# Kernel tuning notes

Hardware: AMD Instinct MI355X
Metric: run time of the kernel (lower is better)

Reference implementation:

```python
import jax, jax.numpy as jnp
import numpy as np


def l2norm(t, eps=1e-12):
    return t / jnp.clip(jnp.linalg.norm(t, axis=-1, keepdims=True), eps, None)


def setup_inputs() -> dict:
    key = jax.random.key(0)
    k1, k2 = jax.random.split(key)
    x = jax.random.normal(k1, (16, 2048, 512), dtype=jnp.float32)
    # codebook: module inits with l2norm(uniform_init(...)); random normals then l2norm is equivalent in spirit
    embed = l2norm(jax.random.normal(k2, (1, 8192, 512), dtype=jnp.float32))
    return {"x": x, "embed": embed}


def reference(x, embed):
    # x: [b, n, d] (ndim < 4 -> add codebook dim h=1), embed: [h, c, d]
    xh = x[None]                                  # [1, b, n, d]
    h, b, n, d = xh.shape
    flatten = l2norm(xh.reshape(h, b * n, d))     # [h, bn, d]
    embed_n = l2norm(embed)                       # [h, c, d]
    # cosine-similarity distances
    dist = jnp.einsum('hnd,hcd->hnc', flatten, embed_n)   # [h, bn, c]
    # sample_codebook_temp = 0 -> gumbel_sample degenerates to argmax
    embed_ind = jnp.argmax(dist, axis=-1).reshape(h, b, n)  # [h, b, n]
    # batched_embedding: gather from the UN-normalized codebook
    quantize = jnp.take_along_axis(embed[:, None], embed_ind[..., None, None].repeat(1, 0), axis=2) if False else embed[jnp.arange(h)[:, None, None], embed_ind]  # [h, b, n, d]
    return quantize[0], embed_ind[0]
```

## Files before the change

### kernel.cpp

```cpp
#include <hip/hip_runtime.h>
#include <math.h>

#define D 512
#define MROWS 32768
#define CCOLS 8192
#define K2 1536
#define NT 24
#define NSPLIT 2
#define CT_PER_SPLIT 16
#define SUBT_PER_CTI (NT * 2)
#define SUBT_TOTAL (CT_PER_SPLIT * SUBT_PER_CTI)
#define TAU 2.0e-4f

typedef __attribute__((ext_vector_type(8))) short short8v;
typedef __attribute__((ext_vector_type(4))) float f32x4;

__device__ __forceinline__ unsigned short f2bf_rne(float f) {
    unsigned u = __float_as_uint(f);
    unsigned r = ((u >> 16) & 1u) + 0x7FFFu;
    return (unsigned short)((u + r) >> 16);
}
__device__ __forceinline__ float bf2f(unsigned short h) {
    return __uint_as_float(((unsigned)h) << 16);
}

__device__ __forceinline__ void gload_lds16(const void* gsrc, void* ldst) {
    __builtin_amdgcn_global_load_lds(
        (const __attribute__((address_space(1))) unsigned int*)gsrc,
        (__attribute__((address_space(3))) unsigned int*)ldst, 16, 0, 0);
}

__global__ __launch_bounds__(64) void prep_embed_kernel(
    const float* __restrict__ embed, unsigned short* __restrict__ E2,
    float* __restrict__ inv_norm) {
    int cb = blockIdx.x, lane = threadIdx.x;
    const float4* r4 = reinterpret_cast<const float4*>(embed + (size_t)cb * D);
    float4 a = r4[lane], b = r4[lane + 64];
    float ss = a.x*a.x + a.y*a.y + a.z*a.z + a.w*a.w
             + b.x*b.x + b.y*b.y + b.z*b.z + b.w*b.w;
#pragma unroll
    for (int off = 32; off > 0; off >>= 1) ss += __shfl_xor(ss, off);
    float inv = 1.0f / fmaxf(sqrtf(ss), 1e-12f);
    if (lane == 0) inv_norm[cb] = inv;
    float ea[4] = {a.x*inv, a.y*inv, a.z*inv, a.w*inv};
    float eb[4] = {b.x*inv, b.y*inv, b.z*inv, b.w*inv};
    ushort4 ha, la, hb, lb;
    { for (int j=0;j<4;++j) (&ha.x)[j] = f2bf_rne(ea[j]); }
    { for (int j=0;j<4;++j) (&la.x)[j] = f2bf_rne(ea[j] - bf2f((&ha.x)[j])); }
    { for (int j=0;j<4;++j) (&hb.x)[j] = f2bf_rne(eb[j]); }
    { for (int j=0;j<4;++j) (&lb.x)[j] = f2bf_rne(eb[j] - bf2f((&hb.x)[j])); }
    unsigned short* row = E2 + (size_t)cb * K2;
    int k = lane * 4;
    *(ushort4*)&row[k]          = ha;
    *(ushort4*)&row[256 + k]    = hb;
    *(ushort4*)&row[512 + k]    = la;
    *(ushort4*)&row[768 + k]    = lb;
    *(ushort4*)&row[1024 + k]   = ha;
    *(ushort4*)&row[1280 + k]   = hb;
}

__global__ __launch_bounds__(64) void prep_x_kernel(
    const float* __restrict__ x, unsigned short* __restrict__ X2) {
    int rb = blockIdx.x, lane = threadIdx.x;
    const float4* r4 = reinterpret_cast<const float4*>(x + (size_t)rb * D);
    float4 a = r4[lane], b = r4[lane + 64];
    float ea[4] = {a.x, a.y, a.z, a.w};
    float eb[4] = {b.x, b.y, b.z, b.w};
    ushort4 ha, la, hb, lb;
    { for (int j=0;j<4;++j) (&ha.x)[j] = f2bf_rne(ea[j]); }
    { for (int j=0;j<4;++j) (&la.x)[j] = f2bf_rne(ea[j] - bf2f((&ha.x)[j])); }
    { for (int j=0;j<4;++j) (&hb.x)[j] = f2bf_rne(eb[j]); }
    { for (int j=0;j<4;++j) (&lb.x)[j] = f2bf_rne(eb[j] - bf2f((&hb.x)[j])); }
    unsigned short* row = X2 + (size_t)rb * K2;
    int k = lane * 4;
    *(ushort4*)&row[k]        = ha;
    *(ushort4*)&row[256 + k]  = hb;
    *(ushort4*)&row[512 + k]  = ha;
    *(ushort4*)&row[768 + k]  = hb;
    *(ushort4*)&row[1024 + k] = la;
    *(ushort4*)&row[1280 + k] = lb;
}

__global__ __launch_bounds__(512, 2) void gemm_topk5_kernel(
    const unsigned short* __restrict__ X2, const unsigned short* __restrict__ E2,
    float4* __restrict__ partials) {
    __shared__ __align__(16) unsigned short AsR[4][256 * 32];
    __shared__ __align__(16) unsigned short BsR[4][256 * 32];
    __shared__ float smv1[256], smv2[256];
    __shared__ int   smi[256];

    const int tid  = threadIdx.x;
    const int lane = tid & 63;
    const int w    = tid >> 6;
    const int wm   = w >> 1;
    const int wn   = w & 1;
    const int c    = lane & 15;
    const int qh   = lane >> 4;

    const int bid     = blockIdx.x;
    const int logical = (bid & 7) * 32 + (bid >> 3);
    const int split   = logical >> 7;
    const int rowtile = logical & 127;
    const size_t grow0 = (size_t)rowtile * 256;
    const int col0     = split * (CT_PER_SPLIT * 256);

    float v1[16], v2[16]; int i1[16];
#pragma unroll
    for (int s = 0; s < 16; ++s) { v1[s] = -3.0e38f; v2[s] = -3.0e38f; i1[s] = 0; }

#define STAGE_SUBT(S)                                                         \
    { int cti_ = (S) / SUBT_PER_CTI;                                          \
      int rem_ = (S) - cti_ * SUBT_PER_CTI;                                   \
      int kb_  = (rem_ >> 1) * 64 + (rem_ & 1) * 32;                          \
      int ct_  = col0 + cti_ * 256;                                           \
      int sl_  = (S) & 3;                                                     \
      _Pragma("unroll")                                                       \
      for (int i_ = 0; i_ < 2; ++i_) {                                        \
          int G_ = tid + i_ * 512; int row_ = G_ >> 2;                        \
          int gs_ = (G_ & 3) ^ ((row_ >> 1) & 3);                             \
          gload_lds16(X2 + (grow0 + row_) * (size_t)K2 + kb_ + gs_ * 8,       \
                      &AsR[sl_][G_ * 8]);                                     \
      }                                                                       \
      _Pragma("unroll")                                                       \
      for (int i_ = 0; i_ < 2; ++i_) {                                        \
          int G_ = tid + i_ * 512; int row_ = G_ >> 2;                        \
          int gs_ = (G_ & 3) ^ ((row_ >> 1) & 3);                             \
          gload_lds16(E2 + (size_t)(ct_ + row_) * K2 + kb_ + gs_ * 8,         \
                      &BsR[sl_][G_ * 8]);                                     \
      } }

    STAGE_SUBT(0);
    STAGE_SUBT(1);
    STAGE_SUBT(2);
    asm volatile("s_waitcnt vmcnt(8)" ::: "memory");

    int sgi = 0;
    for (int cti = 0; cti < CT_PER_SPLIT; ++cti) {
        const int ct0 = col0 + cti * 256;
        f32x4 acc[4][8];
#pragma unroll
        for (int m = 0; m < 4; ++m)
#pragma unroll
            for (int n = 0; n < 8; ++n) acc[m][n] = (f32x4){0.f, 0.f, 0.f, 0.f};

#pragma unroll 4
        for (int s = 0; s < SUBT_PER_CTI; ++s, ++sgi) {
            const int slot = sgi & 3;
            __builtin_amdgcn_s_barrier();
            __builtin_amdgcn_sched_barrier(0);

            short8v af[4], bf[4];
#pragma unroll
            for (int m = 0; m < 4; ++m) {
                int row = wm * 64 + m * 16 + c;
                int g   = qh ^ ((row >> 1) & 3);
                af[m] = *(const short8v*)&AsR[slot][row * 32 + g * 8];
            }
#pragma unroll
            for (int n = 0; n < 4; ++n) {
                int rb = wn * 128 + n * 16 + c;
                int g  = qh ^ ((rb >> 1) & 3);
                bf[n] = *(const short8v*)&BsR[slot][rb * 32 + g * 8];
            }
            __builtin_amdgcn_s_setprio(1);
#pragma unroll
            for (int m = 0; m < 4; ++m)
#pragma unroll
                for (int n = 0; n < 4; ++n)
                    acc[m][n] = __builtin_amdgcn_mfma_f32_16x16x32_bf16(
                        af[m], bf[n], acc[m][n], 0, 0, 0);
            __builtin_amdgcn_s_setprio(0);
#pragma unroll
            for (int n = 0; n < 4; ++n) {
                int rb = wn * 128 + (n + 4) * 16 + c;
                int g  = qh ^ ((rb >> 1) & 3);
                bf[n] = *(const short8v*)&BsR[slot][rb * 32 + g * 8];
            }
            __builtin_amdgcn_s_setprio(1);
#pragma unroll
            for (int m = 0; m < 4; ++m)
#pragma unroll
                for (int n = 0; n < 4; ++n)
                    acc[m][n + 4] = __builtin_amdgcn_mfma_f32_16x16x32_bf16(
                        af[m], bf[n], acc[m][n + 4], 0, 0, 0);
            __builtin_amdgcn_s_setprio(0);

            if (sgi + 3 < SUBT_TOTAL) {
                STAGE_SUBT(sgi + 3);
                asm volatile("s_waitcnt vmcnt(8)" ::: "memory");
            } else if (sgi == SUBT_TOTAL - 3) {
                asm volatile("s_waitcnt vmcnt(4)" ::: "memory");
            } else if (sgi == SUBT_TOTAL - 2) {
                asm volatile("s_waitcnt vmcnt(0)" ::: "memory");
            }
        }

#pragma unroll
        for (int m = 0; m < 4; ++m)
#pragma unroll
            for (int n = 0; n < 8; ++n) {
                int col = ct0 + wn * 128 + n * 16 + c;
#pragma unroll
                for (int r = 0; r < 4; ++r) {
                    float sv = acc[m][n][r];
                    int slot2 = m * 4 + r;
                    if (sv > v1[slot2]) { v2[slot2] = v1[slot2]; v1[slot2] = sv; i1[slot2] = col; }
                    else if (sv > v2[slot2]) v2[slot2] = sv;
                }
            }
    }
#undef STAGE_SUBT

#pragma unroll
    for (int s = 0; s < 16; ++s) {
        float a1 = v1[s], a2 = v2[s]; int ai = i1[s];
#pragma unroll
        for (int off = 1; off < 16; off <<= 1) {
            float o1 = __shfl_xor(a1, off);
            float o2 = __shfl_xor(a2, off);
            int   oi = __shfl_xor(ai, off);
            if (o1 > a1 || (o1 == a1 && oi < ai)) {
                a2 = fmaxf(a1, o2); a1 = o1; ai = oi;
            } else {
                a2 = fmaxf(a2, o1);
            }
        }
        v1[s] = a1; v2[s] = a2; i1[s] = ai;
    }
    if (c == 0 && wn == 1) {
#pragma unroll
        for (int s = 0; s < 16; ++s) {
            int li = wm * 64 + qh * 16 + s;
            smv1[li] = v1[s]; smv2[li] = v2[s]; smi[li] = i1[s];
        }
    }
    __syncthreads();
    if (c == 0 && wn == 0) {
#pragma unroll
        for (int s = 0; s < 16; ++s) {
            int li = wm * 64 + qh * 16 + s;
            float o1 = smv1[li], o2 = smv2[li]; int oi = smi[li];
            if (o1 > v1[s] || (o1 == v1[s] && oi < i1[s])) {
                v2[s] = fmaxf(v1[s], o2); v1[s] = o1; i1[s] = oi;
            } else {
                v2[s] = fmaxf(v2[s], o1);
            }
            int row = (int)grow0 + wm * 64 + (s >> 2) * 16 + qh * 4 + (s & 3);
            partials[(size_t)row * 4 + split] =
                make_float4(v1[s], v2[s], __int_as_float(i1[s]), 0.f);
        }
    }
}

__global__ __launch_bounds__(256) void combine_kernel(
    const float4* __restrict__ partials, int* __restrict__ ind,
    int* __restrict__ fb_count, int* __restrict__ fb_rows,
    unsigned long long* __restrict__ best) {
    int row = blockIdx.x * 256 + threadIdx.x;
    if (row >= MROWS) return;
    float g1 = -3.0e38f, g2 = -3.0e38f; int gi = 0;
#pragma unroll
    for (int s = 0; s < NSPLIT; ++s) {
        float4 p = partials[(size_t)row * 4 + s];
        if (p.x > g1 || (p.x == g1 && __float_as_int(p.z) < gi)) {
            g2 = fmaxf(g1, p.y); g1 = p.x; gi = __float_as_int(p.z);
        } else {
            g2 = fmaxf(g2, p.x);
        }
    }
    ind[row] = gi;
    if (g1 - g2 <= TAU) {
        int k = atomicAdd(fb_count, 1);
        fb_rows[k] = row;
        best[row] = 0ull;
    }
}

__global__ __launch_bounds__(256) void fallback_kernel(
    const float* __restrict__ x, const float* __restrict__ embed,
    const float* __restrict__ inv_norm, const int* __restrict__ fb_count,
    const int* __restrict__ fb_rows, unsigned long long* __restrict__ best) {
    __shared__ float es[16][D];
    __shared__ float xs[D];
    const int t = threadIdx.x;
    const int c0 = blockIdx.x * 16;
    for (int i = t; i < 16 * 128; i += 256) {
        int col = i >> 7, f4 = i & 127;
        *(float4*)&es[col][f4 * 4] =
            *(const float4*)&embed[(size_t)(c0 + col) * D + f4 * 4];
    }
    const int nfb = *fb_count;
    const int col = t >> 4, s = t & 15;
    for (int ri = 0; ri < nfb; ++ri) {
        int row = fb_rows[ri];
        __syncthreads();
        if (t < 128)
            *(float4*)&xs[t * 4] = *(const float4*)&x[(size_t)row * D + t * 4];
        __syncthreads();
        float dot = 0.f;
        const float* ep = &es[col][s * 32];
        const float* xp = &xs[s * 32];
#pragma unroll
        for (int k = 0; k < 8; ++k) {
            float4 a = *(const float4*)&xp[k * 4];
            float4 b = *(const float4*)&ep[k * 4];
            dot = fmaf(a.x, b.x, fmaf(a.y, b.y, fmaf(a.z, b.z, fmaf(a.w, b.w, dot))));
        }
        dot += __shfl_xor(dot, 1); dot += __shfl_xor(dot, 2);
        dot += __shfl_xor(dot, 4); dot += __shfl_xor(dot, 8);
        if (s == 0) {
            float score = dot * inv_norm[c0 + col];
            unsigned fb = __float_as_uint(score);
            fb = (fb & 0x80000000u) ? ~fb : (fb | 0x80000000u);
            unsigned long long key = ((unsigned long long)fb << 32) |
                (unsigned long long)(0xFFFFFFFFu - (unsigned)(c0 + col));
            atomicMax(best + row, key);
        }
    }
}

__global__ void fbwrite_kernel(const int* __restrict__ fb_count,
                               const int* __restrict__ fb_rows,
                               const unsigned long long* __restrict__ best,
                               int* __restrict__ ind) {
    int n = *fb_count;
    for (int i = threadIdx.x; i < n; i += 256) {
        int row = fb_rows[i];
        unsigned long long k = best[row];
        ind[row] = (int)(0xFFFFFFFFu - (unsigned)(k & 0xFFFFFFFFull));
    }
}

__global__ __launch_bounds__(128) void gather_kernel(
    const float* __restrict__ embed, const int* __restrict__ ind,
    float* __restrict__ out_q, float* __restrict__ out_i) {
    int row = blockIdx.x;
    int t = threadIdx.x;
    int idx = ind[row];
    const float4* src = reinterpret_cast<const float4*>(embed + (size_t)idx * D);
    float4* dst = reinterpret_cast<float4*>(out_q + (size_t)row * D);
    dst[t] = src[t];
    if (t == 0) out_i[row] = (float)idx;
}

#define BM 64
#define BN 128
#define BK 32
#define LDX (BM + 4)
#define LDE (BN + 4)

__global__ __launch_bounds__(64) void norm_kernel(const float* __restrict__ embed,
                                                  float* __restrict__ inv_norm) {
    int cb = blockIdx.x, lane = threadIdx.x;
    const float4* r4 = reinterpret_cast<const float4*>(embed + (size_t)cb * D);
    float4 a = r4[lane], b = r4[lane + 64];
    float s = a.x*a.x + a.y*a.y + a.z*a.z + a.w*a.w
            + b.x*b.x + b.y*b.y + b.z*b.z + b.w*b.w;
#pragma unroll
    for (int off = 32; off > 0; off >>= 1) s += __shfl_xor(s, off);
    if (lane == 0) inv_norm[cb] = 1.0f / fmaxf(sqrtf(s), 1e-12f);
}

__global__ __launch_bounds__(256) void gemm_argmax_kernel(
    const float* __restrict__ x, const float* __restrict__ embed,
    const float* __restrict__ inv_norm, int* __restrict__ ind, int C) {
    __shared__ float xs[BK][LDX];
    __shared__ float es[BK][LDE];
    const int tid = threadIdx.x;
    const int tx = tid & 15;
    const int ty = tid >> 4;
    const int row0 = blockIdx.x * BM;
    float bestv[4]; int besti[4];
#pragma unroll
    for (int i = 0; i < 4; ++i) { bestv[i] = -3.0e38f; besti[i] = 0; }
    for (int ct = 0; ct < C; ct += BN) {
        float acc[4][8];
#pragma unroll
        for (int i = 0; i < 4; ++i)
#pragma unroll
            for (int j = 0; j < 8; ++j) acc[i][j] = 0.0f;
        for (int kt = 0; kt < D; kt += BK) {
#pragma unroll
            for (int i = 0; i < 2; ++i) {
                int f = tid + i * 256;
                int r = f >> 3, kq = (f & 7) << 2;
                float4 v = *reinterpret_cast<const float4*>(
                    x + (size_t)(row0 + r) * D + kt + kq);
                xs[kq+0][r]=v.x; xs[kq+1][r]=v.y; xs[kq+2][r]=v.z; xs[kq+3][r]=v.w;
            }
#pragma unroll
            for (int i = 0; i < 4; ++i) {
                int f = tid + i * 256;
                int r = f >> 3, kq = (f & 7) << 2;
                float4 v = *reinterpret_cast<const float4*>(
                    embed + (size_t)(ct + r) * D + kt + kq);
                es[kq+0][r]=v.x; es[kq+1][r]=v.y; es[kq+2][r]=v.z; es[kq+3][r]=v.w;
            }
            __syncthreads();
#pragma unroll
            for (int k = 0; k < BK; ++k) {
                float4 a4 = *reinterpret_cast<const float4*>(&xs[k][ty * 4]);
                float4 b0 = *reinterpret_cast<const float4*>(&es[k][tx * 8]);
                float4 b1 = *reinterpret_cast<const float4*>(&es[k][tx * 8 + 4]);
                float a[4] = {a4.x, a4.y, a4.z, a4.w};
                float b[8] = {b0.x, b0.y, b0.z, b0.w, b1.x, b1.y, b1.z, b1.w};
#pragma unroll
                for (int i = 0; i < 4; ++i)
#pragma unroll
                    for (int j = 0; j < 8; ++j)
                        acc[i][j] = fmaf(a[i], b[j], acc[i][j]);
            }
            __syncthreads();
        }
#pragma unroll
        for (int i = 0; i < 4; ++i) {
            float v = -3.0e38f; int vi = 0;
#pragma unroll
            for (int j = 0; j < 8; ++j) {
                int col = ct + tx * 8 + j;
                float s = acc[i][j] * inv_norm[col];
                if (s > v) { v = s; vi = col; }
            }
#pragma unroll
            for (int off = 1; off < 16; off <<= 1) {
                float ov = __shfl_xor(v, off, 16);
                int   oi = __shfl_xor(vi, off, 16);
                if (ov > v || (ov == v && oi < vi)) { v = ov; vi = oi; }
            }
            if (v > bestv[i] || (v == bestv[i] && vi < besti[i])) {
                bestv[i] = v; besti[i] = vi;
            }
        }
    }
    if (tx == 0) {
#pragma unroll
        for (int i = 0; i < 4; ++i) ind[row0 + ty * 4 + i] = besti[i];
    }
}

extern "C" void kernel_launch(void* const* d_in, const int* in_sizes, int n_in,
                              void* d_out, int out_size, void* d_ws, size_t ws_size,
                              hipStream_t stream) {
    const float* x     = (const float*)d_in[0];
    const float* embed = (const float*)d_in[1];
    const int M = in_sizes[0] / D;
    const int C = in_sizes[1] / D;

    float* out_q = (float*)d_out;
    float* out_i = (float*)d_out + (size_t)M * D;

    size_t X2_off   = 0;
    size_t X2_sz    = (size_t)M * K2 * 2;
    size_t E2_off   = X2_off + X2_sz;
    size_t E2_sz    = (size_t)C * K2 * 2;
    size_t inv_off  = E2_off + E2_sz;
    size_t inv_sz   = (size_t)C * 4;
    size_t part_off = inv_off + inv_sz;
    size_t part_sz  = (size_t)M * 4 * 16;
    size_t ind_off  = part_off + part_sz;
    size_t ind_sz   = (size_t)M * 4;
    size_t fbc_off  = ind_off + ind_sz;
    size_t fbr_off  = fbc_off + 16;
    size_t fbr_sz   = (size_t)M * 4;
    size_t best_off = fbr_off + fbr_sz;
    size_t total    = best_off + (size_t)M * 8;

    if (ws_size >= total && M == MROWS && C == CCOLS) {
        char* ws = (char*)d_ws;
        unsigned short* X2 = (unsigned short*)(ws + X2_off);
        unsigned short* E2 = (unsigned short*)(ws + E2_off);
        float* inv_norm    = (float*)(ws + inv_off);
        float4* partials   = (float4*)(ws + part_off);
        int* ind           = (int*)(ws + ind_off);
        int* fb_count      = (int*)(ws + fbc_off);
        int* fb_rows       = (int*)(ws + fbr_off);
        unsigned long long* best = (unsigned long long*)(ws + best_off);

        hipMemsetAsync(fb_count, 0, 16, stream);
        prep_embed_kernel<<<C, 64, 0, stream>>>(embed, E2, inv_norm);
        prep_x_kernel<<<M, 64, 0, stream>>>(x, X2);
        gemm_topk5_kernel<<<(M / 256) * NSPLIT, 512, 0, stream>>>(X2, E2, partials);
        combine_kernel<<<M / 256, 256, 0, stream>>>(partials, ind, fb_count, fb_rows, best);
        fallback_kernel<<<C / 16, 256, 0, stream>>>(x, embed, inv_norm, fb_count, fb_rows, best);
        fbwrite_kernel<<<1, 256, 0, stream>>>(fb_count, fb_rows, best, ind);
        gather_kernel<<<M, 128, 0, stream>>>(embed, ind, out_q, out_i);
    } else {
        float* inv_norm = (float*)d_ws;
        int*   ind      = (int*)d_ws + C;
        norm_kernel<<<C, 64, 0, stream>>>(embed, inv_norm);
        gemm_argmax_kernel<<<M / BM, 256, 0, stream>>>(x, embed, inv_norm, ind, C);
        gather_kernel<<<M, 128, 0, stream>>>(embed, ind, out_q, out_i);
    }
}
```

Baseline: 1.159 ms.

## Process two K-subtiles per barrier with paired prefetch in GEMM argmax kernel

Reworks the main GEMM loop to consume two LDS subtiles per iteration between barriers, halving the barrier count. Both subtiles two steps ahead are issued together, followed by a full vmcnt(0) wait after the compute. This replaces the rolling three-stage prefetch that issued one stage per step and waited with vmcnt(8). The intent is to cut barrier and wait overhead. The risk is that a full drain each iteration leaves less room to hide load latency behind compute.

```diff
diff --git a/kernel.cpp b/kernel.cpp
--- a/kernel.cpp
+++ b/kernel.cpp
@@ -81,7 +81,7 @@
     *(ushort4*)&row[1280 + k] = lb;
 }
 
-__global__ __launch_bounds__(512, 2) void gemm_topk5_kernel(
+__global__ __launch_bounds__(512, 2) void gemm_topk6_kernel(
     const unsigned short* __restrict__ X2, const unsigned short* __restrict__ E2,
     float4* __restrict__ partials) {
     __shared__ __align__(16) unsigned short AsR[4][256 * 32];
@@ -129,10 +129,48 @@
                       &BsR[sl_][G_ * 8]);                                     \
       } }
 
+#define SUBT_BODY(SLOT)                                                       \
+    {                                                                         \
+        short8v af[4], bf[4];                                                 \
+        _Pragma("unroll")                                                     \
+        for (int m = 0; m < 4; ++m) {                                         \
+            int row = wm * 64 + m * 16 + c;                                   \
+            int g   = qh ^ ((row >> 1) & 3);                                  \
+            af[m] = *(const short8v*)&AsR[SLOT][row * 32 + g * 8];            \
+        }                                                                     \
+        _Pragma("unroll")                                                     \
+        for (int n = 0; n < 4; ++n) {                                         \
+            int rb = wn * 128 + n * 16 + c;                                   \
+            int g  = qh ^ ((rb >> 1) & 3);                                    \
+            bf[n] = *(const short8v*)&BsR[SLOT][rb * 32 + g * 8];             \
+        }                                                                     \
+        __builtin_amdgcn_s_setprio(1);                                        \
+        _Pragma("unroll")                                                     \
+        for (int m = 0; m < 4; ++m)                                           \
+            _Pragma("unroll")                                                 \
+            for (int n = 0; n < 4; ++n)                                       \
+                acc[m][n] = __builtin_amdgcn_mfma_f32_16x16x32_bf16(          \
+                    af[m], bf[n], acc[m][n], 0, 0, 0);                        \
+        __builtin_amdgcn_s_setprio(0);                                        \
+        _Pragma("unroll")                                                     \
+        for (int n = 0; n < 4; ++n) {                                         \
+            int rb = wn * 128 + (n + 4) * 16 + c;                             \
+            int g  = qh ^ ((rb >> 1) & 3);                                    \
+            bf[n] = *(const short8v*)&BsR[SLOT][rb * 32 + g * 8];             \
+        }                                                                     \
+        __builtin_amdgcn_s_setprio(1);                                        \
+        _Pragma("unroll")                                                     \
+        for (int m = 0; m < 4; ++m)                                           \
+            _Pragma("unroll")                                                 \
+            for (int n = 0; n < 4; ++n)                                       \
+                acc[m][n + 4] = __builtin_amdgcn_mfma_f32_16x16x32_bf16(      \
+                    af[m], bf[n], acc[m][n + 4], 0, 0, 0);                    \
+        __builtin_amdgcn_s_setprio(0);                                        \
+    }
+
     STAGE_SUBT(0);
     STAGE_SUBT(1);
-    STAGE_SUBT(2);
-    asm volatile("s_waitcnt vmcnt(8)" ::: "memory");
+    asm volatile("s_waitcnt vmcnt(0)" ::: "memory");
 
     int sgi = 0;
     for (int cti = 0; cti < CT_PER_SPLIT; ++cti) {
@@ -143,56 +181,22 @@
 #pragma unroll
             for (int n = 0; n < 8; ++n) acc[m][n] = (f32x4){0.f, 0.f, 0.f, 0.f};
 
-#pragma unroll 4
-        for (int s = 0; s < SUBT_PER_CTI; ++s, ++sgi) {
-            const int slot = sgi & 3;
+#pragma unroll 2
+        for (int s = 0; s < SUBT_PER_CTI; s += 2, sgi += 2) {
+            const int slot0 = sgi & 3;
+            const int slot1 = (sgi + 1) & 3;
             __builtin_amdgcn_s_barrier();
             __builtin_amdgcn_sched_barrier(0);
 
-            short8v af[4], bf[4];
-#pragma unroll
-            for (int m = 0; m < 4; ++m) {
-                int row = wm * 64 + m * 16 + c;
-                int g   = qh ^ ((row >> 1) & 3);
-                af[m] = *(const short8v*)&AsR[slot][row * 32 + g * 8];
-            }
-#pragma unroll
-            for (int n = 0; n < 4; ++n) {
-                int rb = wn * 128 + n * 16 + c;
-                int g  = qh ^ ((rb >> 1) & 3);
-                bf[n] = *(const short8v*)&BsR[slot][rb * 32 + g * 8];
-            }
-            __builtin_amdgcn_s_setprio(1);
-#pragma unroll
-            for (int m = 0; m < 4; ++m)
-#pragma unroll
-                for (int n = 0; n < 4; ++n)
-                    acc[m][n] = __builtin_amdgcn_mfma_f32_16x16x32_bf16(
-                        af[m], bf[n], acc[m][n], 0, 0, 0);
-            __builtin_amdgcn_s_setprio(0);
-#pragma unroll
-            for (int n = 0; n < 4; ++n) {
-                int rb = wn * 128 + (n + 4) * 16 + c;
-                int g  = qh ^ ((rb >> 1) & 3);
-                bf[n] = *(const short8v*)&BsR[slot][rb * 32 + g * 8];
-            }
-            __builtin_amdgcn_s_setprio(1);
-#pragma unroll
-            for (int m = 0; m < 4; ++m)
-#pragma unroll
-                for (int n = 0; n < 4; ++n)
-                    acc[m][n + 4] = __builtin_amdgcn_mfma_f32_16x16x32_bf16(
-                        af[m], bf[n], acc[m][n + 4], 0, 0, 0);
-            __builtin_amdgcn_s_setprio(0);
-
             if (sgi + 3 < SUBT_TOTAL) {
+                STAGE_SUBT(sgi + 2);
                 STAGE_SUBT(sgi + 3);
-                asm volatile("s_waitcnt vmcnt(8)" ::: "memory");
-            } else if (sgi == SUBT_TOTAL - 3) {
-                asm volatile("s_waitcnt vmcnt(4)" ::: "memory");
-            } else if (sgi == SUBT_TOTAL - 2) {
-                asm volatile("s_waitcnt vmcnt(0)" ::: "memory");
-            }
+            }
+
+            SUBT_BODY(slot0);
+            SUBT_BODY(slot1);
+
+            asm volatile("s_waitcnt vmcnt(0)" ::: "memory");
         }
 
 #pragma unroll
@@ -209,6 +213,7 @@
                 }
             }
     }
+#undef SUBT_BODY
 #undef STAGE_SUBT
 
 #pragma unroll
@@ -479,7 +484,7 @@
         hipMemsetAsync(fb_count, 0, 16, stream);
         prep_embed_kernel<<<C, 64, 0, stream>>>(embed, E2, inv_norm);
         prep_x_kernel<<<M, 64, 0, stream>>>(x, X2);
-        gemm_topk5_kernel<<<(M / 256) * NSPLIT, 512, 0, stream>>>(X2, E2, partials);
+        gemm_topk6_kernel<<<(M / 256) * NSPLIT, 512, 0, stream>>>(X2, E2, partials);
         combine_kernel<<<M / 256, 256, 0, stream>>>(partials, ind, fb_count, fb_rows, best);
         fallback_kernel<<<C / 16, 256, 0, stream>>>(x, embed, inv_norm, fb_count, fb_rows, best);
         fbwrite_kernel<<<1, 256, 0, stream>>>(fb_count, fb_rows, best, ind);
```

New measurement: 1.240 ms. +6.9%, slower.
